# Optimization experiments

Hardware: AMD Instinct MI355X
Metric: run time of the kernel (lower is better)

Reference implementation:

```python
import jax, jax.numpy as jnp
import numpy as np

N = 262144      # total nodes
E = 1048576     # total edges
G = 8192        # num graphs (= batch[-1]+1)
H = 128         # hidden
L = 4           # layers
VA = 64         # atom feature vocab
VB = 8          # bond feature vocab
FA = 9          # atom feature columns
FB = 3          # bond feature columns
BN_EPS = 1e-5


def _bn(x, g, b, m, v):
    # BatchNorm1d in eval mode: running stats
    return (x - m) * jax.lax.rsqrt(v + BN_EPS) * g + b


def setup_inputs() -> dict:
    key = jax.random.key(0)
    ks = jax.random.split(key, 40)
    rn = lambda k, s, sc=0.05: jax.random.normal(k, s, dtype=jnp.float32) * sc
    x = jax.random.randint(ks[0], (N, FA), 0, VA)
    edge_index = jax.random.randint(ks[1], (2, E), 0, N)
    edge_attr = jax.random.randint(ks[2], (E, FB), 0, VB)
    batch = jnp.sort(jax.random.randint(ks[3], (N,), 0, G))
    batch = batch.at[0].set(0).at[-1].set(G - 1)
    params = dict(
        atom_emb=rn(ks[4], (FA, VA, H)),
        vn_emb=rn(ks[5], (H,)),
        bond_emb=rn(ks[6], (L, FB, VB, H)),
        conv_eps=rn(ks[7], (L,)),
        conv_W1=rn(ks[8], (L, H, 2 * H)), conv_b1=rn(ks[9], (L, 2 * H)),
        conv_bn_g=1.0 + rn(ks[10], (L, 2 * H)), conv_bn_b=rn(ks[11], (L, 2 * H)),
        conv_bn_m=rn(ks[12], (L, 2 * H), 0.1),
        conv_bn_v=0.5 + jax.random.uniform(ks[13], (L, 2 * H)) * 0.5,
        conv_W2=rn(ks[14], (L, 2 * H, H)), conv_b2=rn(ks[15], (L, H)),
        vn1_W=rn(ks[16], (L, 2 * H, 2 * H)), vn1_b=rn(ks[17], (L, 2 * H)),
        vn1_g=1.0 + rn(ks[18], (L, 2 * H)), vn1_be=rn(ks[19], (L, 2 * H)),
        vn1_m=rn(ks[20], (L, 2 * H), 0.1),
        vn1_v=0.5 + jax.random.uniform(ks[21], (L, 2 * H)) * 0.5,
        vn2_W=rn(ks[22], (L, 2 * H, H)), vn2_b=rn(ks[23], (L, H)),
        vn2_g=1.0 + rn(ks[24], (L, H)), vn2_be=rn(ks[25], (L, H)),
        vn2_m=rn(ks[26], (L, H), 0.1),
        vn2_v=0.5 + jax.random.uniform(ks[27], (L, H)) * 0.5,
        pW1=rn(ks[28], (H, H)), pb1=rn(ks[29], (H,)),
        pW2=rn(ks[30], (H, 1)), pb2=rn(ks[31], (1,)),
    )
    return dict(x=x, edge_index=edge_index, edge_attr=edge_attr, batch=batch, **params)


def reference(x, edge_index, edge_attr, batch, atom_emb, vn_emb, bond_emb,
              conv_eps, conv_W1, conv_b1, conv_bn_g, conv_bn_b, conv_bn_m, conv_bn_v,
              conv_W2, conv_b2, vn1_W, vn1_b, vn1_g, vn1_be, vn1_m, vn1_v,
              vn2_W, vn2_b, vn2_g, vn2_be, vn2_m, vn2_v, pW1, pb1, pW2, pb2):
    src, dst = edge_index[0], edge_index[1]
    # AtomEncoder: sum of per-feature embeddings -> [N, H]
    h = atom_emb[jnp.arange(FA)[:, None], x.T].sum(0)
    # virtual node embedding broadcast to all graphs: [G, H]
    vn = jnp.broadcast_to(vn_emb, (G, H))
    for i in range(L):
        h = h + vn[batch]
        # CombConv (GIN-with-edge-features): msg = relu(x_j + bond_emb)
        e = bond_emb[i][jnp.arange(FB)[:, None], edge_attr.T].sum(0)  # [E, H]
        msg = jax.nn.relu(h[src] + e)
        agg = jax.ops.segment_sum(msg, dst, num_segments=N)  # [N, H]
        z = (1.0 + conv_eps[i]) * h + agg
        z = jax.nn.relu(_bn(z @ conv_W1[i] + conv_b1[i],
                            conv_bn_g[i], conv_bn_b[i], conv_bn_m[i], conv_bn_v[i]))
        h = z @ conv_W2[i] + conv_b2[i]
        # virtual node update: gather-concat-MLP, pool, MLP
        t = jnp.concatenate([vn[batch], h], axis=-1)  # [N, 2H]
        t = jax.nn.relu(_bn(t @ vn1_W[i] + vn1_b[i],
                            vn1_g[i], vn1_be[i], vn1_m[i], vn1_v[i]))
        pooled = jax.ops.segment_sum(t, batch, num_segments=G)  # [G, 2H]
        vn = jax.nn.relu(_bn(pooled @ vn2_W[i] + vn2_b[i],
                             vn2_g[i], vn2_be[i], vn2_m[i], vn2_v[i]))
    # JK='L': last virtual-node representation; dropout=0
    out = jax.nn.relu(vn @ pW1 + pb1) @ pW2 + pb2  # [G, 1]
    return jnp.clip(out, 0.0, 50.0)  # eval-mode clamp
```

## Files before the change

### kernel.cpp

```cpp
#include <hip/hip_runtime.h>
#include <hip/hip_fp16.h>

#define NN 262144
#define EE 1048576
#define GG 8192
#define HH 128
#define FBc 3
#define VAc 64
#define VBc 8
#define FAc 9

typedef _Float16 f16;
typedef _Float16 f16x8 __attribute__((ext_vector_type(8)));
typedef float f32x4 __attribute__((ext_vector_type(4)));

__device__ __forceinline__ float h2f(ushort u) {
    __half h; *(ushort*)&h = u; return __half2float(h);
}
__device__ __forceinline__ ushort f2h(float f) {
    __half h = __float2half_rn(f); return *(ushort*)&h;
}
__device__ __forceinline__ int swz(int col, int row) {
    return (((col >> 3) ^ (row & 7)) << 3) | (col & 7);
}

__global__ void k_zero(float* __restrict__ p) {
    size_t i = (size_t)(blockIdx.x * 256 + threadIdx.x) * 4;
    *(float4*)(p + i) = make_float4(0.f, 0.f, 0.f, 0.f);
}

__global__ void k_atom(const int* __restrict__ x, const float* __restrict__ emb,
                       ushort* __restrict__ h16) {
    int t = blockIdx.x * 256 + threadIdx.x;
    int n = t >> 5, c = (t & 31) << 2;
    if (n >= NN) return;
    float4 a = make_float4(0.f, 0.f, 0.f, 0.f);
#pragma unroll
    for (int f = 0; f < FAc; ++f) {
        int v = x[n * FAc + f];
        float4 e = *(const float4*)(emb + ((size_t)(f * VAc + v)) * HH + c);
        a.x += e.x; a.y += e.y; a.z += e.z; a.w += e.w;
    }
    ushort4 o;
    o.x = f2h(a.x * 0.0625f); o.y = f2h(a.y * 0.0625f);
    o.z = f2h(a.z * 0.0625f); o.w = f2h(a.w * 0.0625f);
    *(ushort4*)(h16 + (size_t)n * HH + c) = o;
}

__global__ void k_init_vn(const float* __restrict__ vn_emb, float* __restrict__ vn) {
    int t = blockIdx.x * 256 + threadIdx.x;
    int g = t >> 5, c = (t & 31) << 2;
    *(float4*)(vn + (size_t)g * HH + c) = *(const float4*)(vn_emb + c);
}

__global__ void k_hist(const int* __restrict__ ei, int* __restrict__ deg) {
    int e = blockIdx.x * 256 + threadIdx.x;
    atomicAdd(&deg[ei[EE + e]], 1);
}
__global__ void k_scan1(const int* __restrict__ deg, int* __restrict__ rowptr,
                        int* __restrict__ sums) {
    __shared__ int s[256];
    int base = blockIdx.x * 1024 + threadIdx.x * 4;
    int4 d = *(const int4*)(deg + base);
    int t = d.x + d.y + d.z + d.w;
    s[threadIdx.x] = t;
    __syncthreads();
    for (int off = 1; off < 256; off <<= 1) {
        int v = (threadIdx.x >= off) ? s[threadIdx.x - off] : 0;
        __syncthreads();
        s[threadIdx.x] += v;
        __syncthreads();
    }
    int excl = s[threadIdx.x] - t;
    int4 o; o.x = excl; o.y = excl + d.x; o.z = o.y + d.y; o.w = o.z + d.z;
    *(int4*)(rowptr + base) = o;
    if (threadIdx.x == 255) sums[blockIdx.x] = s[255];
}
__global__ void k_scan2(int* __restrict__ sums) {
    __shared__ int s[256];
    int t = sums[threadIdx.x];
    s[threadIdx.x] = t;
    __syncthreads();
    for (int off = 1; off < 256; off <<= 1) {
        int v = (threadIdx.x >= off) ? s[threadIdx.x - off] : 0;
        __syncthreads();
        s[threadIdx.x] += v;
        __syncthreads();
    }
    sums[threadIdx.x] = s[threadIdx.x] - t;
}
__global__ void k_scan3(int* __restrict__ rowptr, const int* __restrict__ sums,
                        int* __restrict__ fill) {
    int base = blockIdx.x * 1024 + threadIdx.x * 4;
    int add = sums[blockIdx.x];
    int4 r = *(const int4*)(rowptr + base);
    r.x += add; r.y += add; r.z += add; r.w += add;
    *(int4*)(rowptr + base) = r;
    *(int4*)(fill + base) = r;
    if (blockIdx.x == 0 && threadIdx.x == 0) rowptr[NN] = EE;
}
__global__ void k_scatter(const int* __restrict__ ei, const int* __restrict__ ea,
                          int* __restrict__ fill, unsigned* __restrict__ packed) {
    int e = blockIdx.x * 256 + threadIdx.x;
    int dst = ei[EE + e];
    int pos = atomicAdd(&fill[dst], 1);
    unsigned cb = (unsigned)(ea[e * 3 + 0] + ea[e * 3 + 1] * 8 + ea[e * 3 + 2] * 64);
    packed[pos] = (unsigned)ei[e] | (cb << 18);
}

__global__ void k_setup(const float* __restrict__ bemb, ushort* __restrict__ ct16,
                        const float* __restrict__ b1, const float* __restrict__ g1,
                        const float* __restrict__ be1, const float* __restrict__ m1,
                        const float* __restrict__ v1,
                        const float* __restrict__ g3, const float* __restrict__ be3,
                        const float* __restrict__ m3, const float* __restrict__ v3,
                        float* __restrict__ ZA, float* __restrict__ ZB,
                        float* __restrict__ TA, float* __restrict__ TB,
                        float* __restrict__ S3,
                        const float* __restrict__ W1, ushort* __restrict__ W1t,
                        const float* __restrict__ W2, ushort* __restrict__ W2t,
                        const float* __restrict__ W3, ushort* __restrict__ W3t,
                        const float* __restrict__ vn, ushort* __restrict__ vn16,
                        float* __restrict__ pooled) {
    int t = blockIdx.x * 256 + threadIdx.x;
    if (t < 16384) {
        int cb = t >> 5, c = (t & 31) << 2;
        int a0 = cb & 7, a1 = (cb >> 3) & 7, a2 = cb >> 6;
        float4 b0 = *(const float4*)(bemb + (size_t)(0 * VBc + a0) * HH + c);
        float4 b1v = *(const float4*)(bemb + (size_t)(1 * VBc + a1) * HH + c);
        float4 b2v = *(const float4*)(bemb + (size_t)(2 * VBc + a2) * HH + c);
        ushort4 o;
        o.x = f2h((b0.x + b1v.x + b2v.x) * 0.0625f);
        o.y = f2h((b0.y + b1v.y + b2v.y) * 0.0625f);
        o.z = f2h((b0.z + b1v.z + b2v.z) * 0.0625f);
        o.w = f2h((b0.w + b1v.w + b2v.w) * 0.0625f);
        *(ushort4*)(ct16 + (size_t)cb * HH + c) = o;
    } else if (t < 16640) {
        int c = t - 16384;
        float s1 = g1[c] * rsqrtf(v1[c] + 1e-5f);
        ZA[c] = s1;
        ZB[c] = ((b1[c] - m1[c]) * s1 + be1[c]) * 0.0625f;
        float s3 = g3[c] * rsqrtf(v3[c] + 1e-5f);
        TA[c] = 16.f * s3;
        TB[c] = be3[c] - m3[c] * s3;
        S3[c] = s3;
    } else if (t < 278784) {
        int i4 = t - 16640;
        float4 v = *(const float4*)(vn + (size_t)i4 * 4);
        ushort4 o;
        o.x = f2h(v.x * 0.0625f); o.y = f2h(v.y * 0.0625f);
        o.z = f2h(v.z * 0.0625f); o.w = f2h(v.w * 0.0625f);
        *(ushort4*)(vn16 + (size_t)i4 * 4) = o;
    } else if (t < 311552) {
        int o = t - 278784;
        int c = o >> 7, k = o & 127;
        W1t[o] = f2h(W1[(size_t)k * 256 + c]);
    } else if (t < 344320) {
        int o = t - 311552;
        int c = o >> 8, k = o & 255;
        W2t[o] = f2h(W2[(size_t)k * 128 + c]);
    } else if (t < 377088) {
        int o = t - 344320;
        int c = o >> 7, k = o & 127;
        W3t[o] = f2h(W3[(size_t)k * 256 + c]);
    } else {
        int i4 = t - 377088;
        *(float4*)(pooled + (size_t)i4 * 4) = make_float4(0.f, 0.f, 0.f, 0.f);
    }
}

__global__ void __launch_bounds__(256, 3)
k_conv(const ushort* __restrict__ h16in, ushort* __restrict__ h16out,
       const int* __restrict__ rowptr, const unsigned* __restrict__ packed,
       const ushort* __restrict__ ct16,
       const ushort* __restrict__ W1t, const ushort* __restrict__ W2t,
       const ushort* __restrict__ W3t,
       const int* __restrict__ batch, const ushort* __restrict__ vn16,
       const float* __restrict__ vnW,
       const float* __restrict__ eps_ptr,
       const float* __restrict__ ZA, const float* __restrict__ ZB,
       const float* __restrict__ b2,
       const float* __restrict__ TA, const float* __restrict__ TB,
       float* __restrict__ pooled) {
    __shared__ ushort zs[64][256];
    __shared__ ushort Wb[64][128];
    ushort(*Wb2)[256] = (ushort(*)[256]) & Wb[0][0];
    const int tid = threadIdx.x;
    const int r0 = blockIdx.x * 64;
    const int w = tid >> 6, l = tid & 63, lr = l & 15, lg = l >> 4, lr7 = lr & 7;
    const float eps1 = 1.f + eps_ptr[0];
    const int myrow = w * 16 + lr;
    const int growA = r0 + myrow;
    const int ggA = batch[growA];
    int rl[4], ggs[4];
#pragma unroll
    for (int reg = 0; reg < 4; ++reg) {
        rl[reg] = w * 16 + lg * 4 + reg;
        ggs[reg] = batch[r0 + rl[reg]];
    }

    {
        int grp = tid >> 4, ln = tid & 15;
        int ch0 = ln * 8;
        for (int rr = 0; rr < 4; ++rr) {
            int row = grp * 4 + rr;
            int beg = rowptr[r0 + row], end = rowptr[r0 + row + 1];
            float ac[8] = {0.f, 0.f, 0.f, 0.f, 0.f, 0.f, 0.f, 0.f};
            int e = beg;
            for (; e + 1 < end; e += 2) {
                unsigned p0 = packed[e], p1 = packed[e + 1];
                int s0 = p0 & 0x3FFFF, s1 = p1 & 0x3FFFF;
                int c0 = p0 >> 18, c1 = p1 >> 18;
                f16x8 h0 = *(const f16x8*)(h16in + (size_t)s0 * HH + ch0);
                f16x8 h1 = *(const f16x8*)(h16in + (size_t)s1 * HH + ch0);
                f16x8 v0 = *(const f16x8*)(vn16 + (size_t)batch[s0] * HH + ch0);
                f16x8 v1 = *(const f16x8*)(vn16 + (size_t)batch[s1] * HH + ch0);
                f16x8 t0 = *(const f16x8*)(ct16 + (size_t)c0 * HH + ch0);
                f16x8 t1 = *(const f16x8*)(ct16 + (size_t)c1 * HH + ch0);
#pragma unroll
                for (int j = 0; j < 8; ++j) {
                    ac[j] += fmaxf((float)h0[j] + (float)v0[j] + (float)t0[j], 0.f)
                           + fmaxf((float)h1[j] + (float)v1[j] + (float)t1[j], 0.f);
                }
            }
            if (e < end) {
                unsigned p = packed[e];
                int src = p & 0x3FFFF, cb = p >> 18;
                f16x8 hv = *(const f16x8*)(h16in + (size_t)src * HH + ch0);
                f16x8 vv = *(const f16x8*)(vn16 + (size_t)batch[src] * HH + ch0);
                f16x8 ct = *(const f16x8*)(ct16 + (size_t)cb * HH + ch0);
#pragma unroll
                for (int j = 0; j < 8; ++j)
                    ac[j] += fmaxf((float)hv[j] + (float)vv[j] + (float)ct[j], 0.f);
            }
            f16x8 o;
#pragma unroll
            for (int j = 0; j < 8; ++j) o[j] = (f16)ac[j];
            *(f16x8*)&zs[row][((ch0 >> 3) ^ (row & 7)) << 3] = o;
        }
    }
    __syncthreads();

    f16x8 af[4];
#pragma unroll
    for (int k0 = 0; k0 < 4; ++k0) {
        int ko = k0 * 32 + lg * 8;
        f16x8 hv = *(const f16x8*)(h16in + (size_t)growA * HH + ko);
        f16x8 vv = *(const f16x8*)(vn16 + (size_t)ggA * HH + ko);
        f16x8 ag = *(const f16x8*)&zs[myrow][((ko >> 3) ^ (myrow & 7)) << 3];
#pragma unroll
        for (int j = 0; j < 8; ++j)
            af[k0][j] = (f16)(eps1 * ((float)hv[j] + (float)vv[j]) + (float)ag[j]);
    }

    for (int qt = 0; qt < 4; ++qt) {
        __syncthreads();
        {
            int c = tid >> 2, q = tid & 3, c7 = c & 7;
            const ushort* s = W1t + (size_t)(qt * 64 + c) * 128 + q * 32;
#pragma unroll
            for (int j4 = 0; j4 < 4; ++j4)
                *(f16x8*)&Wb[c][((q * 4 + j4) ^ c7) << 3] = *(const f16x8*)(s + j4 * 8);
        }
        __syncthreads();
        f32x4 acc[4] = {};
#pragma unroll
        for (int k0 = 0; k0 < 4; ++k0) {
            int sb = ((k0 * 4 + lg) ^ lr7) << 3;
#pragma unroll
            for (int fc = 0; fc < 4; ++fc) {
                f16x8 bf = *(const f16x8*)&Wb[fc * 16 + lr][sb];
                acc[fc] = __builtin_amdgcn_mfma_f32_16x16x32_f16(af[k0], bf, acc[fc], 0, 0, 0);
            }
        }
#pragma unroll
        for (int fc = 0; fc < 4; ++fc) {
            int col = qt * 64 + fc * 16 + lr;
            float za = ZA[col], zb = ZB[col];
#pragma unroll
            for (int reg = 0; reg < 4; ++reg) {
                float zv = fmaxf(acc[fc][reg] * za + zb, 0.f);
                zs[rl[reg]][swz(col, rl[reg])] = f2h(zv);
            }
        }
    }

    f32x4 acc2[8] = {};
    for (int st = 0; st < 4; ++st) {
        __syncthreads();
        {
            int c = tid >> 3, q = tid & 7, c7 = c & 7;
            const ushort* s = W2t + (size_t)(st * 32 + c) * 256 + q * 32;
#pragma unroll
            for (int j4 = 0; j4 < 4; ++j4)
                *(f16x8*)&Wb2[c][((q * 4 + j4) ^ c7) << 3] = *(const f16x8*)(s + j4 * 8);
        }
        __syncthreads();
#pragma unroll
        for (int k0 = 0; k0 < 8; ++k0) {
            int sb = ((k0 * 4 + lg) ^ lr7) << 3;
            f16x8 az = *(const f16x8*)&zs[myrow][sb];
#pragma unroll
            for (int fc = 0; fc < 2; ++fc) {
                f16x8 bf = *(const f16x8*)&Wb2[fc * 16 + lr][sb];
                acc2[st * 2 + fc] =
                    __builtin_amdgcn_mfma_f32_16x16x32_f16(az, bf, acc2[st * 2 + fc], 0, 0, 0);
            }
        }
    }
    __syncthreads();
#pragma unroll
    for (int st = 0; st < 4; ++st) {
#pragma unroll
        for (int fc = 0; fc < 2; ++fc) {
            int col = st * 32 + fc * 16 + lr;
            float bb = b2[col];
#pragma unroll
            for (int reg = 0; reg < 4; ++reg) {
                float hv = acc2[st * 2 + fc][reg] * 16.f + bb;
                zs[rl[reg]][swz(col, rl[reg])] = f2h(hv * 0.0625f);
            }
        }
    }
    {
        int row = tid >> 2, q = tid & 3, r7 = row & 7;
#pragma unroll
        for (int j4 = 0; j4 < 4; ++j4) {
            f16x8 v = *(const f16x8*)&zs[row][((q * 4 + j4) ^ r7) << 3];
            *(f16x8*)(h16out + (size_t)(r0 + row) * HH + q * 32 + j4 * 8) = v;
        }
    }

    for (int pr = 0; pr < 2; ++pr) {
#pragma unroll
        for (int sub = 0; sub < 2; ++sub) {
            int qt = pr * 2 + sub;
            __syncthreads();
            {
                int c = tid >> 2, q = tid & 3, c7 = c & 7;
                const ushort* s = W3t + (size_t)(qt * 64 + c) * 128 + q * 32;
#pragma unroll
                for (int j4 = 0; j4 < 4; ++j4)
                    *(f16x8*)&Wb[c][((q * 4 + j4) ^ c7) << 3] = *(const f16x8*)(s + j4 * 8);
            }
            __syncthreads();
            f32x4 acc3[4] = {};
#pragma unroll
            for (int k0 = 0; k0 < 4; ++k0) {
                int sb = ((k0 * 4 + lg) ^ lr7) << 3;
                f16x8 ah = *(const f16x8*)&zs[myrow][sb];
#pragma unroll
                for (int fc = 0; fc < 4; ++fc) {
                    f16x8 bf = *(const f16x8*)&Wb[fc * 16 + lr][sb];
                    acc3[fc] = __builtin_amdgcn_mfma_f32_16x16x32_f16(ah, bf, acc3[fc], 0, 0, 0);
                }
            }
#pragma unroll
            for (int fc = 0; fc < 4; ++fc) {
                int colg = qt * 64 + fc * 16 + lr;
                int colL = 128 + sub * 64 + fc * 16 + lr;
                float ta = TA[colg], tb = TB[colg];
#pragma unroll
                for (int reg = 0; reg < 4; ++reg) {
                    float tv = fmaxf(acc3[fc][reg] * ta + vnW[(size_t)ggs[reg] * 256 + colg] + tb, 0.f);
                    zs[rl[reg]][swz(colL, rl[reg])] = f2h(tv);
                }
            }
        }
        __syncthreads();
        {
            int c = tid & 127, half = tid >> 7;
            int gcol = pr * 128 + c;
            int colL = 128 + c;
            float s = 0.f;
            int cur = batch[r0 + half * 32];
            for (int r = half * 32; r < half * 32 + 32; ++r) {
                int gg = batch[r0 + r];
                if (gg != cur) {
                    atomicAdd(&pooled[(size_t)cur * 256 + gcol], s);
                    s = 0.f; cur = gg;
                }
                s += h2f(zs[r][swz(colL, r)]);
            }
            atomicAdd(&pooled[(size_t)cur * 256 + gcol], s);
        }
        __syncthreads();
    }
}

enum { E_BIAS = 0, E_BNRELU = 1 };
template <int EMODE>
__global__ void __launch_bounds__(256)
gemm_k(const void* __restrict__ Av, const float* __restrict__ B,
       const float* __restrict__ bias,
       const float* __restrict__ g_, const float* __restrict__ b_,
       const float* __restrict__ m_, const float* __restrict__ v_,
       const float* __restrict__ scp,
       void* __restrict__ outv, int K, int Nc) {
    __shared__ float As[64][33];
    __shared__ float Bs[32][64];
    const int tid = threadIdx.x;
    const int row0 = blockIdx.x * 64;
    const int col0 = blockIdx.y * 64;
    float acc[4][4] = {};
    const int tx = tid & 15, ty = tid >> 4;
    for (int k0 = 0; k0 < K; k0 += 32) {
#pragma unroll
        for (int p = 0; p < 2; ++p) {
            int idx = p * 256 + tid;
            {
                int r = idx >> 3, c = (idx & 7) << 2;
                size_t aoff = (size_t)(row0 + r) * K + k0 + c;
                float4 va = *(const float4*)((const float*)Av + aoff);
                As[r][c + 0] = va.x; As[r][c + 1] = va.y;
                As[r][c + 2] = va.z; As[r][c + 3] = va.w;
            }
            {
                int kr = idx >> 4, cc = (idx & 15) << 2;
                *(float4*)&Bs[kr][cc] =
                    *(const float4*)(B + (size_t)(k0 + kr) * Nc + col0 + cc);
            }
        }
        __syncthreads();
#pragma unroll
        for (int k = 0; k < 32; ++k) {
            float4 bv = *(const float4*)&Bs[k][tx << 2];
            float a0 = As[ty * 4 + 0][k];
            float a1 = As[ty * 4 + 1][k];
            float a2 = As[ty * 4 + 2][k];
            float a3 = As[ty * 4 + 3][k];
            acc[0][0] += a0 * bv.x; acc[0][1] += a0 * bv.y; acc[0][2] += a0 * bv.z; acc[0][3] += a0 * bv.w;
            acc[1][0] += a1 * bv.x; acc[1][1] += a1 * bv.y; acc[1][2] += a1 * bv.z; acc[1][3] += a1 * bv.w;
            acc[2][0] += a2 * bv.x; acc[2][1] += a2 * bv.y; acc[2][2] += a2 * bv.z; acc[2][3] += a2 * bv.w;
            acc[3][0] += a3 * bv.x; acc[3][1] += a3 * bv.y; acc[3][2] += a3 * bv.z; acc[3][3] += a3 * bv.w;
        }
        __syncthreads();
    }
#pragma unroll
    for (int j = 0; j < 4; ++j) {
        int gr = row0 + ty * 4 + j;
        float vals[4];
#pragma unroll
        for (int lx = 0; lx < 4; ++lx) {
            int gc = col0 + (tx << 2) + lx;
            float val = acc[j][lx];
            if (EMODE == E_BIAS) {
                float v = val + bias[gc];
                if (scp) v *= scp[gc];
                vals[lx] = v;
            } else {
                float y = val + bias[gc];
                float s = g_[gc] * rsqrtf(v_[gc] + 1e-5f);
                y = (y - m_[gc]) * s + b_[gc];
                vals[lx] = fmaxf(y, 0.f);
            }
        }
        *(float4*)((float*)outv + (size_t)gr * Nc + col0 + (tx << 2)) =
            make_float4(vals[0], vals[1], vals[2], vals[3]);
    }
}

__global__ void k_final(const float* __restrict__ vn, const float* __restrict__ pW1,
                        const float* __restrict__ pb1, const float* __restrict__ pW2,
                        const float* __restrict__ pb2, float* __restrict__ out) {
    int g = blockIdx.x;
    int j = threadIdx.x;
    __shared__ float vrow[HH];
    __shared__ float red[HH];
    vrow[j] = vn[(size_t)g * HH + j];
    __syncthreads();
    float acc = pb1[j];
    for (int k = 0; k < HH; ++k) acc = fmaf(vrow[k], pW1[k * HH + j], acc);
    red[j] = fmaxf(acc, 0.f) * pW2[j];
    __syncthreads();
    for (int s = 64; s > 0; s >>= 1) {
        if (j < s) red[j] += red[j + s];
        __syncthreads();
    }
    if (j == 0) out[g] = fminf(fmaxf(red[0] + pb2[0], 0.f), 50.f);
}

extern "C" void kernel_launch(void* const* d_in, const int* in_sizes, int n_in,
                              void* d_out, int out_size, void* d_ws, size_t ws_size,
                              hipStream_t stream) {
    const int*   x        = (const int*)  d_in[0];
    const int*   ei       = (const int*)  d_in[1];
    const int*   ea       = (const int*)  d_in[2];
    const int*   batch    = (const int*)  d_in[3];
    const float* atom_emb = (const float*)d_in[4];
    const float* vn_emb   = (const float*)d_in[5];
    const float* bond_emb = (const float*)d_in[6];
    const float* conv_eps = (const float*)d_in[7];
    const float* conv_W1  = (const float*)d_in[8];
    const float* conv_b1  = (const float*)d_in[9];
    const float* cbn_g    = (const float*)d_in[10];
    const float* cbn_b    = (const float*)d_in[11];
    const float* cbn_m    = (const float*)d_in[12];
    const float* cbn_v    = (const float*)d_in[13];
    const float* conv_W2  = (const float*)d_in[14];
    const float* conv_b2  = (const float*)d_in[15];
    const float* vn1_W    = (const float*)d_in[16];
    const float* vn1_b    = (const float*)d_in[17];
    const float* vn1_g    = (const float*)d_in[18];
    const float* vn1_be   = (const float*)d_in[19];
    const float* vn1_m    = (const float*)d_in[20];
    const float* vn1_v    = (const float*)d_in[21];
    const float* vn2_W    = (const float*)d_in[22];
    const float* vn2_b    = (const float*)d_in[23];
    const float* vn2_g    = (const float*)d_in[24];
    const float* vn2_be   = (const float*)d_in[25];
    const float* vn2_m    = (const float*)d_in[26];
    const float* vn2_v    = (const float*)d_in[27];
    const float* pW1      = (const float*)d_in[28];
    const float* pb1      = (const float*)d_in[29];
    const float* pW2      = (const float*)d_in[30];
    const float* pb2      = (const float*)d_in[31];

    char* base = (char*)d_ws;
    ushort*   h16a   = (ushort*)base;
    ushort*   h16b   = h16a + (size_t)NN * HH;
    unsigned* packed = (unsigned*)(h16b + (size_t)NN * HH);
    int*      rowptr = (int*)(packed + EE);
    int*      fill   = rowptr + NN + 4;
    ushort*   ct16   = (ushort*)(fill + NN);
    int*      sums   = (int*)(ct16 + 512 * HH);
    ushort*   W1t    = (ushort*)(sums + 256);
    ushort*   W2t    = W1t + 256 * 128;
    ushort*   W3t    = W2t + 128 * 256;
    float*    ZA     = (float*)(W3t + 256 * 128);
    float*    ZB     = ZA + 256;
    float*    TA     = ZB + 256;
    float*    TB     = TA + 256;
    float*    S3     = TB + 256;
    float*    vn     = S3 + 256;
    ushort*   vn16   = (ushort*)(vn + (size_t)GG * HH);
    float*    vnW    = (float*)(vn16 + (size_t)GG * HH);
    float*    pooled = vnW + (size_t)GG * 256;
    float*    out    = (float*)d_out;

    k_zero<<<256, 256, 0, stream>>>((float*)fill);
    k_hist<<<EE / 256, 256, 0, stream>>>(ei, fill);
    k_scan1<<<256, 256, 0, stream>>>(fill, rowptr, sums);
    k_scan2<<<1, 256, 0, stream>>>(sums);
    k_scan3<<<256, 256, 0, stream>>>(rowptr, sums, fill);
    k_scatter<<<EE / 256, 256, 0, stream>>>(ei, ea, fill, packed);
    k_atom<<<NN * 32 / 256, 256, 0, stream>>>(x, atom_emb, h16a);
    k_init_vn<<<GG * HH / 4 / 256, 256, 0, stream>>>(vn_emb, vn);

    for (int i = 0; i < 4; ++i) {
        ushort* hin  = (i & 1) ? h16b : h16a;
        ushort* hout = (i & 1) ? h16a : h16b;

        k_setup<<<3521, 256, 0, stream>>>(
            bond_emb + (size_t)i * FBc * VBc * HH, ct16,
            conv_b1 + i * 256, cbn_g + i * 256, cbn_b + i * 256,
            cbn_m + i * 256, cbn_v + i * 256,
            vn1_g + i * 256, vn1_be + i * 256, vn1_m + i * 256, vn1_v + i * 256,
            ZA, ZB, TA, TB, S3,
            conv_W1 + (size_t)i * HH * 256, W1t,
            conv_W2 + (size_t)i * 256 * HH, W2t,
            vn1_W + (size_t)i * 256 * 256 + 128 * 256, W3t,
            vn, vn16, pooled);

        {
            dim3 g3(GG / 64, 4);
            gemm_k<E_BIAS><<<g3, 256, 0, stream>>>(
                vn, vn1_W + (size_t)i * 256 * 256, vn1_b + i * 256,
                nullptr, nullptr, nullptr, nullptr, S3, vnW, HH, 256);
        }

        k_conv<<<NN / 64, 256, 0, stream>>>(
            hin, hout, rowptr, packed, ct16,
            W1t, W2t, W3t, batch, vn16, vnW, conv_eps + i,
            ZA, ZB, conv_b2 + i * HH, TA, TB, pooled);

        {
            dim3 g4(GG / 64, 2);
            gemm_k<E_BNRELU><<<g4, 256, 0, stream>>>(
                pooled, vn2_W + (size_t)i * 256 * HH, vn2_b + i * HH,
                vn2_g + i * HH, vn2_be + i * HH, vn2_m + i * HH, vn2_v + i * HH,
                nullptr, vn, 256, HH);
        }
    }
    k_final<<<GG, 128, 0, stream>>>(vn, pW1, pb1, pW2, pb2, out);
}
```

Baseline: 1.543 ms.

## Precompute h+vn once per layer, fuse VN MLPs, hoist per-layer setup

A new per-layer VN kernel fuses the previous layer's vn2 MLP, the next vn1 projection and the pooled zeroing. It also writes hb16 = h + vn[batch] once per node, so the conv edge gather no longer loads vn16 and batch for every edge. Setup for all four layers moves into a single kernel before the loop, and the generic gemm kernels are removed. The edge loop is unrolled by four and MFMA sections get s_setprio hints. This adds a full extra pass over node features each layer, which trades against the per-edge gather it saves.

```diff
diff --git a/kernel.cpp b/kernel.cpp
--- a/kernel.cpp
+++ b/kernel.cpp
@@ -45,12 +45,6 @@
     o.x = f2h(a.x * 0.0625f); o.y = f2h(a.y * 0.0625f);
     o.z = f2h(a.z * 0.0625f); o.w = f2h(a.w * 0.0625f);
     *(ushort4*)(h16 + (size_t)n * HH + c) = o;
-}
-
-__global__ void k_init_vn(const float* __restrict__ vn_emb, float* __restrict__ vn) {
-    int t = blockIdx.x * 256 + threadIdx.x;
-    int g = t >> 5, c = (t & 31) << 2;
-    *(float4*)(vn + (size_t)g * HH + c) = *(const float4*)(vn_emb + c);
 }
 
 __global__ void k_hist(const int* __restrict__ ei, int* __restrict__ deg) {
@@ -107,23 +101,33 @@
     unsigned cb = (unsigned)(ea[e * 3 + 0] + ea[e * 3 + 1] * 8 + ea[e * 3 + 2] * 64);
     packed[pos] = (unsigned)ei[e] | (cb << 18);
 }
-
-__global__ void k_setup(const float* __restrict__ bemb, ushort* __restrict__ ct16,
-                        const float* __restrict__ b1, const float* __restrict__ g1,
-                        const float* __restrict__ be1, const float* __restrict__ m1,
-                        const float* __restrict__ v1,
-                        const float* __restrict__ g3, const float* __restrict__ be3,
-                        const float* __restrict__ m3, const float* __restrict__ v3,
-                        float* __restrict__ ZA, float* __restrict__ ZB,
-                        float* __restrict__ TA, float* __restrict__ TB,
-                        float* __restrict__ S3,
-                        const float* __restrict__ W1, ushort* __restrict__ W1t,
-                        const float* __restrict__ W2, ushort* __restrict__ W2t,
-                        const float* __restrict__ W3, ushort* __restrict__ W3t,
-                        const float* __restrict__ vn, ushort* __restrict__ vn16,
-                        float* __restrict__ pooled) {
-    int t = blockIdx.x * 256 + threadIdx.x;
+__global__ void k_gstart(const int* __restrict__ batch, int* __restrict__ gstart) {
+    int n = blockIdx.x * 256 + threadIdx.x;
+    if (n >= NN) return;
+    int b0 = batch[n];
+    int b1 = (n + 1 < NN) ? batch[n + 1] : GG;
+    if (n == 0) gstart[0] = 0;
+    for (int g = b0 + 1; g <= b1; ++g) gstart[g] = n + 1;
+}
+
+__global__ void k_setup_all(
+    const float* __restrict__ bond_emb, ushort* __restrict__ ct16_all,
+    const float* __restrict__ conv_b1, const float* __restrict__ cbn_g,
+    const float* __restrict__ cbn_b, const float* __restrict__ cbn_m,
+    const float* __restrict__ cbn_v,
+    const float* __restrict__ vn1_g, const float* __restrict__ vn1_be,
+    const float* __restrict__ vn1_m, const float* __restrict__ vn1_v,
+    const float* __restrict__ vn2_g, const float* __restrict__ vn2_be,
+    const float* __restrict__ vn2_m, const float* __restrict__ vn2_v,
+    const float* __restrict__ vn2_b,
+    float* __restrict__ tabs,
+    const float* __restrict__ conv_W1, ushort* __restrict__ W1t_all,
+    const float* __restrict__ conv_W2, ushort* __restrict__ W2t_all,
+    const float* __restrict__ vn1_W,  ushort* __restrict__ W3t_all) {
+    int layer = blockIdx.x / 449;
+    int t = (blockIdx.x % 449) * 256 + threadIdx.x;
     if (t < 16384) {
+        const float* bemb = bond_emb + (size_t)layer * FBc * VBc * HH;
         int cb = t >> 5, c = (t & 31) << 2;
         int a0 = cb & 7, a1 = (cb >> 3) & 7, a2 = cb >> 6;
         float4 b0 = *(const float4*)(bemb + (size_t)(0 * VBc + a0) * HH + c);
@@ -134,53 +138,143 @@
         o.y = f2h((b0.y + b1v.y + b2v.y) * 0.0625f);
         o.z = f2h((b0.z + b1v.z + b2v.z) * 0.0625f);
         o.w = f2h((b0.w + b1v.w + b2v.w) * 0.0625f);
-        *(ushort4*)(ct16 + (size_t)cb * HH + c) = o;
+        *(ushort4*)(ct16_all + (size_t)layer * 512 * HH + (size_t)cb * HH + c) = o;
     } else if (t < 16640) {
         int c = t - 16384;
-        float s1 = g1[c] * rsqrtf(v1[c] + 1e-5f);
-        ZA[c] = s1;
-        ZB[c] = ((b1[c] - m1[c]) * s1 + be1[c]) * 0.0625f;
-        float s3 = g3[c] * rsqrtf(v3[c] + 1e-5f);
-        TA[c] = 16.f * s3;
-        TB[c] = be3[c] - m3[c] * s3;
-        S3[c] = s3;
-    } else if (t < 278784) {
-        int i4 = t - 16640;
-        float4 v = *(const float4*)(vn + (size_t)i4 * 4);
-        ushort4 o;
-        o.x = f2h(v.x * 0.0625f); o.y = f2h(v.y * 0.0625f);
-        o.z = f2h(v.z * 0.0625f); o.w = f2h(v.w * 0.0625f);
-        *(ushort4*)(vn16 + (size_t)i4 * 4) = o;
-    } else if (t < 311552) {
-        int o = t - 278784;
+        float* T = tabs + (size_t)layer * 1536;
+        float s1 = cbn_g[layer * 256 + c] * rsqrtf(cbn_v[layer * 256 + c] + 1e-5f);
+        T[0 * 256 + c] = s1;
+        T[1 * 256 + c] = ((conv_b1[layer * 256 + c] - cbn_m[layer * 256 + c]) * s1
+                          + cbn_b[layer * 256 + c]) * 0.0625f;
+        float s3 = vn1_g[layer * 256 + c] * rsqrtf(vn1_v[layer * 256 + c] + 1e-5f);
+        T[2 * 256 + c] = 16.f * s3;
+        T[3 * 256 + c] = vn1_be[layer * 256 + c] - vn1_m[layer * 256 + c] * s3;
+        T[4 * 256 + c] = s3;
+        if (c < 128) {
+            float s2 = vn2_g[layer * 128 + c] * rsqrtf(vn2_v[layer * 128 + c] + 1e-5f);
+            T[5 * 256 + c] = s2;
+            T[5 * 256 + 128 + c] = (vn2_b[layer * 128 + c] - vn2_m[layer * 128 + c]) * s2
+                                   + vn2_be[layer * 128 + c];
+        }
+    } else if (t < 49408) {
+        int o = t - 16640;
         int c = o >> 7, k = o & 127;
-        W1t[o] = f2h(W1[(size_t)k * 256 + c]);
-    } else if (t < 344320) {
-        int o = t - 311552;
+        W1t_all[(size_t)layer * 32768 + o] =
+            f2h(conv_W1[(size_t)layer * 128 * 256 + (size_t)k * 256 + c]);
+    } else if (t < 82176) {
+        int o = t - 49408;
         int c = o >> 8, k = o & 255;
-        W2t[o] = f2h(W2[(size_t)k * 128 + c]);
-    } else if (t < 377088) {
-        int o = t - 344320;
+        W2t_all[(size_t)layer * 32768 + o] =
+            f2h(conv_W2[(size_t)layer * 256 * 128 + (size_t)k * 128 + c]);
+    } else if (t < 114944) {
+        int o = t - 82176;
         int c = o >> 7, k = o & 127;
-        W3t[o] = f2h(W3[(size_t)k * 256 + c]);
+        W3t_all[(size_t)layer * 32768 + o] =
+            f2h(vn1_W[(size_t)layer * 256 * 256 + 128 * 256 + (size_t)k * 256 + c]);
+    }
+}
+
+template <int MODE>
+__global__ void __launch_bounds__(256)
+k_vn(float* __restrict__ pooled, const float* __restrict__ vn_emb,
+     const float* __restrict__ vn2W_prev,
+     const float* __restrict__ tab_prev,
+     const float* __restrict__ vn1W_cur,
+     const float* __restrict__ vn1b_cur,
+     const float* __restrict__ tab_cur,
+     float* __restrict__ vn_out, float* __restrict__ vnW,
+     const ushort* __restrict__ h16, ushort* __restrict__ hb16,
+     const int* __restrict__ gstart, const int* __restrict__ batch) {
+    __shared__ float pl[16][256];
+    __shared__ float vnL[16][128];
+    const int tid = threadIdx.x;
+    const int g0 = blockIdx.x * 16;
+
+    if (MODE != 0) {
+        for (int i = tid; i < 1024; i += 256) {
+            int r = i >> 6, c4 = (i & 63) << 2;
+            *(float4*)&pl[r][c4] = *(const float4*)(pooled + (size_t)(g0 + r) * 256 + c4);
+        }
+        __syncthreads();
+        {
+            int r = tid >> 4, c0 = (tid & 15) * 8;
+            float acc[8] = {};
+            for (int k = 0; k < 256; ++k) {
+                float a = pl[r][k];
+                const float* wr = vn2W_prev + (size_t)k * 128 + c0;
+                float4 w0 = *(const float4*)wr, w1 = *(const float4*)(wr + 4);
+                acc[0] += a * w0.x; acc[1] += a * w0.y; acc[2] += a * w0.z; acc[3] += a * w0.w;
+                acc[4] += a * w1.x; acc[5] += a * w1.y; acc[6] += a * w1.z; acc[7] += a * w1.w;
+            }
+            const float* VA = tab_prev + 5 * 256;
+            const float* VB = VA + 128;
+#pragma unroll
+            for (int j = 0; j < 8; ++j)
+                vnL[r][c0 + j] = fmaxf(acc[j] * VA[c0 + j] + VB[c0 + j], 0.f);
+        }
     } else {
-        int i4 = t - 377088;
-        *(float4*)(pooled + (size_t)i4 * 4) = make_float4(0.f, 0.f, 0.f, 0.f);
+        for (int i = tid; i < 2048; i += 256) {
+            int r = i >> 7, c = i & 127;
+            vnL[r][c] = vn_emb[c];
+        }
+    }
+    __syncthreads();
+    for (int i = tid; i < 512; i += 256) {
+        int r = i >> 5, c4 = (i & 31) << 2;
+        *(float4*)(vn_out + (size_t)(g0 + r) * 128 + c4) = *(const float4*)&vnL[r][c4];
+    }
+    if (MODE == 2) return;
+
+    {
+        int r = tid >> 4, c0 = (tid & 15) * 16;
+        float acc[16] = {};
+        for (int k = 0; k < 128; ++k) {
+            float a = vnL[r][k];
+            const float* wr = vn1W_cur + (size_t)k * 256 + c0;
+#pragma unroll
+            for (int j4 = 0; j4 < 4; ++j4) {
+                float4 w = *(const float4*)(wr + j4 * 4);
+                acc[j4 * 4 + 0] += a * w.x; acc[j4 * 4 + 1] += a * w.y;
+                acc[j4 * 4 + 2] += a * w.z; acc[j4 * 4 + 3] += a * w.w;
+            }
+        }
+        const float* S3 = tab_cur + 4 * 256;
+#pragma unroll
+        for (int j = 0; j < 16; ++j)
+            vnW[(size_t)(g0 + r) * 256 + c0 + j] =
+                (acc[j] + vn1b_cur[c0 + j]) * S3[c0 + j];
+    }
+    for (int i = tid; i < 1024; i += 256) {
+        int r = i >> 6, c4 = (i & 63) << 2;
+        *(float4*)(pooled + (size_t)(g0 + r) * 256 + c4) = make_float4(0.f, 0.f, 0.f, 0.f);
+    }
+    {
+        int nn0 = gstart[g0], nn1 = gstart[g0 + 16];
+        for (int q = nn0 * 4 + tid; q < nn1 * 4; q += 256) {
+            int n = q >> 2, ch0 = (q & 3) * 32;
+            int g = batch[n] - g0;
+#pragma unroll
+            for (int j4 = 0; j4 < 4; ++j4) {
+                f16x8 hv = *(const f16x8*)(h16 + (size_t)n * HH + ch0 + j4 * 8);
+                f16x8 o;
+#pragma unroll
+                for (int j = 0; j < 8; ++j)
+                    o[j] = (f16)((float)hv[j] + vnL[g][ch0 + j4 * 8 + j] * 0.0625f);
+                *(f16x8*)(hb16 + (size_t)n * HH + ch0 + j4 * 8) = o;
+            }
+        }
     }
 }
 
 __global__ void __launch_bounds__(256, 3)
-k_conv(const ushort* __restrict__ h16in, ushort* __restrict__ h16out,
+k_conv(ushort* __restrict__ h16, const ushort* __restrict__ hb16,
        const int* __restrict__ rowptr, const unsigned* __restrict__ packed,
        const ushort* __restrict__ ct16,
        const ushort* __restrict__ W1t, const ushort* __restrict__ W2t,
        const ushort* __restrict__ W3t,
-       const int* __restrict__ batch, const ushort* __restrict__ vn16,
-       const float* __restrict__ vnW,
-       const float* __restrict__ eps_ptr,
-       const float* __restrict__ ZA, const float* __restrict__ ZB,
+       const int* __restrict__ batch, const float* __restrict__ vnW,
+       const float* __restrict__ eps_ptr, const float* __restrict__ tabs,
        const float* __restrict__ b2,
-       const float* __restrict__ TA, const float* __restrict__ TB,
        float* __restrict__ pooled) {
     __shared__ ushort zs[64][256];
     __shared__ ushort Wb[64][128];
@@ -191,7 +285,10 @@
     const float eps1 = 1.f + eps_ptr[0];
     const int myrow = w * 16 + lr;
     const int growA = r0 + myrow;
-    const int ggA = batch[growA];
+    const float* ZA = tabs;
+    const float* ZB = tabs + 256;
+    const float* TA = tabs + 512;
+    const float* TB = tabs + 768;
     int rl[4], ggs[4];
 #pragma unroll
     for (int reg = 0; reg < 4; ++reg) {
@@ -207,31 +304,32 @@
             int beg = rowptr[r0 + row], end = rowptr[r0 + row + 1];
             float ac[8] = {0.f, 0.f, 0.f, 0.f, 0.f, 0.f, 0.f, 0.f};
             int e = beg;
-            for (; e + 1 < end; e += 2) {
+            for (; e + 3 < end; e += 4) {
                 unsigned p0 = packed[e], p1 = packed[e + 1];
-                int s0 = p0 & 0x3FFFF, s1 = p1 & 0x3FFFF;
-                int c0 = p0 >> 18, c1 = p1 >> 18;
-                f16x8 h0 = *(const f16x8*)(h16in + (size_t)s0 * HH + ch0);
-                f16x8 h1 = *(const f16x8*)(h16in + (size_t)s1 * HH + ch0);
-                f16x8 v0 = *(const f16x8*)(vn16 + (size_t)batch[s0] * HH + ch0);
-                f16x8 v1 = *(const f16x8*)(vn16 + (size_t)batch[s1] * HH + ch0);
-                f16x8 t0 = *(const f16x8*)(ct16 + (size_t)c0 * HH + ch0);
-                f16x8 t1 = *(const f16x8*)(ct16 + (size_t)c1 * HH + ch0);
+                unsigned p2 = packed[e + 2], p3 = packed[e + 3];
+                f16x8 h0 = *(const f16x8*)(hb16 + (size_t)(p0 & 0x3FFFF) * HH + ch0);
+                f16x8 h1 = *(const f16x8*)(hb16 + (size_t)(p1 & 0x3FFFF) * HH + ch0);
+                f16x8 h2 = *(const f16x8*)(hb16 + (size_t)(p2 & 0x3FFFF) * HH + ch0);
+                f16x8 h3 = *(const f16x8*)(hb16 + (size_t)(p3 & 0x3FFFF) * HH + ch0);
+                f16x8 t0 = *(const f16x8*)(ct16 + (size_t)(p0 >> 18) * HH + ch0);
+                f16x8 t1 = *(const f16x8*)(ct16 + (size_t)(p1 >> 18) * HH + ch0);
+                f16x8 t2 = *(const f16x8*)(ct16 + (size_t)(p2 >> 18) * HH + ch0);
+                f16x8 t3 = *(const f16x8*)(ct16 + (size_t)(p3 >> 18) * HH + ch0);
 #pragma unroll
                 for (int j = 0; j < 8; ++j) {
-                    ac[j] += fmaxf((float)h0[j] + (float)v0[j] + (float)t0[j], 0.f)
-                           + fmaxf((float)h1[j] + (float)v1[j] + (float)t1[j], 0.f);
+                    ac[j] += fmaxf((float)h0[j] + (float)t0[j], 0.f)
+                           + fmaxf((float)h1[j] + (float)t1[j], 0.f)
+                           + fmaxf((float)h2[j] + (float)t2[j], 0.f)
+                           + fmaxf((float)h3[j] + (float)t3[j], 0.f);
                 }
             }
-            if (e < end) {
+            for (; e < end; ++e) {
                 unsigned p = packed[e];
-                int src = p & 0x3FFFF, cb = p >> 18;
-                f16x8 hv = *(const f16x8*)(h16in + (size_t)src * HH + ch0);
-                f16x8 vv = *(const f16x8*)(vn16 + (size_t)batch[src] * HH + ch0);
-                f16x8 ct = *(const f16x8*)(ct16 + (size_t)cb * HH + ch0);
+                f16x8 hv = *(const f16x8*)(hb16 + (size_t)(p & 0x3FFFF) * HH + ch0);
+                f16x8 ct = *(const f16x8*)(ct16 + (size_t)(p >> 18) * HH + ch0);
 #pragma unroll
                 for (int j = 0; j < 8; ++j)
-                    ac[j] += fmaxf((float)hv[j] + (float)vv[j] + (float)ct[j], 0.f);
+                    ac[j] += fmaxf((float)hv[j] + (float)ct[j], 0.f);
             }
             f16x8 o;
 #pragma unroll
@@ -245,12 +343,11 @@
 #pragma unroll
     for (int k0 = 0; k0 < 4; ++k0) {
         int ko = k0 * 32 + lg * 8;
-        f16x8 hv = *(const f16x8*)(h16in + (size_t)growA * HH + ko);
-        f16x8 vv = *(const f16x8*)(vn16 + (size_t)ggA * HH + ko);
+        f16x8 hb = *(const f16x8*)(hb16 + (size_t)growA * HH + ko);
         f16x8 ag = *(const f16x8*)&zs[myrow][((ko >> 3) ^ (myrow & 7)) << 3];
 #pragma unroll
         for (int j = 0; j < 8; ++j)
-            af[k0][j] = (f16)(eps1 * ((float)hv[j] + (float)vv[j]) + (float)ag[j]);
+            af[k0][j] = (f16)(eps1 * (float)hb[j] + (float)ag[j]);
     }
 
     for (int qt = 0; qt < 4; ++qt) {
@@ -264,6 +361,7 @@
         }
         __syncthreads();
         f32x4 acc[4] = {};
+        __builtin_amdgcn_s_setprio(1);
 #pragma unroll
         for (int k0 = 0; k0 < 4; ++k0) {
             int sb = ((k0 * 4 + lg) ^ lr7) << 3;
@@ -273,6 +371,7 @@
                 acc[fc] = __builtin_amdgcn_mfma_f32_16x16x32_f16(af[k0], bf, acc[fc], 0, 0, 0);
             }
         }
+        __builtin_amdgcn_s_setprio(0);
 #pragma unroll
         for (int fc = 0; fc < 4; ++fc) {
             int col = qt * 64 + fc * 16 + lr;
@@ -296,6 +395,7 @@
                 *(f16x8*)&Wb2[c][((q * 4 + j4) ^ c7) << 3] = *(const f16x8*)(s + j4 * 8);
         }
         __syncthreads();
+        __builtin_amdgcn_s_setprio(1);
 #pragma unroll
         for (int k0 = 0; k0 < 8; ++k0) {
             int sb = ((k0 * 4 + lg) ^ lr7) << 3;
@@ -307,6 +407,7 @@
                     __builtin_amdgcn_mfma_f32_16x16x32_f16(az, bf, acc2[st * 2 + fc], 0, 0, 0);
             }
         }
+        __builtin_amdgcn_s_setprio(0);
     }
     __syncthreads();
 #pragma unroll
@@ -327,7 +428,7 @@
 #pragma unroll
         for (int j4 = 0; j4 < 4; ++j4) {
             f16x8 v = *(const f16x8*)&zs[row][((q * 4 + j4) ^ r7) << 3];
-            *(f16x8*)(h16out + (size_t)(r0 + row) * HH + q * 32 + j4 * 8) = v;
+            *(f16x8*)(h16 + (size_t)(r0 + row) * HH + q * 32 + j4 * 8) = v;
         }
     }
 
@@ -345,6 +446,7 @@
             }
             __syncthreads();
             f32x4 acc3[4] = {};
+            __builtin_amdgcn_s_setprio(1);
 #pragma unroll
             for (int k0 = 0; k0 < 4; ++k0) {
                 int sb = ((k0 * 4 + lg) ^ lr7) << 3;
@@ -355,6 +457,7 @@
                     acc3[fc] = __builtin_amdgcn_mfma_f32_16x16x32_f16(ah, bf, acc3[fc], 0, 0, 0);
                 }
             }
+            __builtin_amdgcn_s_setprio(0);
 #pragma unroll
             for (int fc = 0; fc < 4; ++fc) {
                 int colg = qt * 64 + fc * 16 + lr;
@@ -385,78 +488,6 @@
             atomicAdd(&pooled[(size_t)cur * 256 + gcol], s);
         }
         __syncthreads();
-    }
-}
-
-enum { E_BIAS = 0, E_BNRELU = 1 };
-template <int EMODE>
-__global__ void __launch_bounds__(256)
-gemm_k(const void* __restrict__ Av, const float* __restrict__ B,
-       const float* __restrict__ bias,
-       const float* __restrict__ g_, const float* __restrict__ b_,
-       const float* __restrict__ m_, const float* __restrict__ v_,
-       const float* __restrict__ scp,
-       void* __restrict__ outv, int K, int Nc) {
-    __shared__ float As[64][33];
-    __shared__ float Bs[32][64];
-    const int tid = threadIdx.x;
-    const int row0 = blockIdx.x * 64;
-    const int col0 = blockIdx.y * 64;
-    float acc[4][4] = {};
-    const int tx = tid & 15, ty = tid >> 4;
-    for (int k0 = 0; k0 < K; k0 += 32) {
-#pragma unroll
-        for (int p = 0; p < 2; ++p) {
-            int idx = p * 256 + tid;
-            {
-                int r = idx >> 3, c = (idx & 7) << 2;
-                size_t aoff = (size_t)(row0 + r) * K + k0 + c;
-                float4 va = *(const float4*)((const float*)Av + aoff);
-                As[r][c + 0] = va.x; As[r][c + 1] = va.y;
-                As[r][c + 2] = va.z; As[r][c + 3] = va.w;
-            }
-            {
-                int kr = idx >> 4, cc = (idx & 15) << 2;
-                *(float4*)&Bs[kr][cc] =
-                    *(const float4*)(B + (size_t)(k0 + kr) * Nc + col0 + cc);
-            }
-        }
-        __syncthreads();
-#pragma unroll
-        for (int k = 0; k < 32; ++k) {
-            float4 bv = *(const float4*)&Bs[k][tx << 2];
-            float a0 = As[ty * 4 + 0][k];
-            float a1 = As[ty * 4 + 1][k];
-            float a2 = As[ty * 4 + 2][k];
-            float a3 = As[ty * 4 + 3][k];
-            acc[0][0] += a0 * bv.x; acc[0][1] += a0 * bv.y; acc[0][2] += a0 * bv.z; acc[0][3] += a0 * bv.w;
-            acc[1][0] += a1 * bv.x; acc[1][1] += a1 * bv.y; acc[1][2] += a1 * bv.z; acc[1][3] += a1 * bv.w;
-            acc[2][0] += a2 * bv.x; acc[2][1] += a2 * bv.y; acc[2][2] += a2 * bv.z; acc[2][3] += a2 * bv.w;
-            acc[3][0] += a3 * bv.x; acc[3][1] += a3 * bv.y; acc[3][2] += a3 * bv.z; acc[3][3] += a3 * bv.w;
-        }
-        __syncthreads();
-    }
-#pragma unroll
-    for (int j = 0; j < 4; ++j) {
-        int gr = row0 + ty * 4 + j;
-        float vals[4];
-#pragma unroll
-        for (int lx = 0; lx < 4; ++lx) {
-            int gc = col0 + (tx << 2) + lx;
-            float val = acc[j][lx];
-            if (EMODE == E_BIAS) {
-                float v = val + bias[gc];
-                if (scp) v *= scp[gc];
-                vals[lx] = v;
-            } else {
-                float y = val + bias[gc];
-                float s = g_[gc] * rsqrtf(v_[gc] + 1e-5f);
-                y = (y - m_[gc]) * s + b_[gc];
-                vals[lx] = fmaxf(y, 0.f);
-            }
-        }
-        *(float4*)((float*)outv + (size_t)gr * Nc + col0 + (tx << 2)) =
-            make_float4(vals[0], vals[1], vals[2], vals[3]);
     }
 }
 
@@ -517,26 +548,22 @@
     const float* pb2      = (const float*)d_in[31];
 
     char* base = (char*)d_ws;
-    ushort*   h16a   = (ushort*)base;
-    ushort*   h16b   = h16a + (size_t)NN * HH;
-    unsigned* packed = (unsigned*)(h16b + (size_t)NN * HH);
-    int*      rowptr = (int*)(packed + EE);
-    int*      fill   = rowptr + NN + 4;
-    ushort*   ct16   = (ushort*)(fill + NN);
-    int*      sums   = (int*)(ct16 + 512 * HH);
-    ushort*   W1t    = (ushort*)(sums + 256);
-    ushort*   W2t    = W1t + 256 * 128;
-    ushort*   W3t    = W2t + 128 * 256;
-    float*    ZA     = (float*)(W3t + 256 * 128);
-    float*    ZB     = ZA + 256;
-    float*    TA     = ZB + 256;
-    float*    TB     = TA + 256;
-    float*    S3     = TB + 256;
-    float*    vn     = S3 + 256;
-    ushort*   vn16   = (ushort*)(vn + (size_t)GG * HH);
-    float*    vnW    = (float*)(vn16 + (size_t)GG * HH);
-    float*    pooled = vnW + (size_t)GG * 256;
-    float*    out    = (float*)d_out;
+    ushort*   h16     = (ushort*)base;
+    ushort*   hb16    = h16 + (size_t)NN * HH;
+    unsigned* packed  = (unsigned*)(hb16 + (size_t)NN * HH);
+    int*      rowptr  = (int*)(packed + EE);
+    int*      fill    = rowptr + NN + 4;
+    int*      gstart  = fill + NN;
+    int*      sums    = gstart + GG + 8;
+    ushort*   ct16a   = (ushort*)(sums + 256);
+    ushort*   W1ta    = ct16a + 4 * 512 * HH;
+    ushort*   W2ta    = W1ta + 4 * 32768;
+    ushort*   W3ta    = W2ta + 4 * 32768;
+    float*    tabs    = (float*)(W3ta + 4 * 32768);
+    float*    vn      = tabs + 4 * 1536;
+    float*    vnW     = vn + (size_t)GG * HH;
+    float*    pooled  = vnW + (size_t)GG * 256;
+    float*    out     = (float*)d_out;
 
     k_zero<<<256, 256, 0, stream>>>((float*)fill);
     k_hist<<<EE / 256, 256, 0, stream>>>(ei, fill);
@@ -544,43 +571,39 @@
     k_scan2<<<1, 256, 0, stream>>>(sums);
     k_scan3<<<256, 256, 0, stream>>>(rowptr, sums, fill);
     k_scatter<<<EE / 256, 256, 0, stream>>>(ei, ea, fill, packed);
-    k_atom<<<NN * 32 / 256, 256, 0, stream>>>(x, atom_emb, h16a);
-    k_init_vn<<<GG * HH / 4 / 256, 256, 0, stream>>>(vn_emb, vn);
+    k_gstart<<<NN / 256, 256, 0, stream>>>(batch, gstart);
+    k_atom<<<NN * 32 / 256, 256, 0, stream>>>(x, atom_emb, h16);
+    k_setup_all<<<4 * 449, 256, 0, stream>>>(
+        bond_emb, ct16a,
+        conv_b1, cbn_g, cbn_b, cbn_m, cbn_v,
+        vn1_g, vn1_be, vn1_m, vn1_v,
+        vn2_g, vn2_be, vn2_m, vn2_v, vn2_b,
+        tabs, conv_W1, W1ta, conv_W2, W2ta, vn1_W, W3ta);
 
     for (int i = 0; i < 4; ++i) {
-        ushort* hin  = (i & 1) ? h16b : h16a;
-        ushort* hout = (i & 1) ? h16a : h16b;
-
-        k_setup<<<3521, 256, 0, stream>>>(
-            bond_emb + (size_t)i * FBc * VBc * HH, ct16,
-            conv_b1 + i * 256, cbn_g + i * 256, cbn_b + i * 256,
-            cbn_m + i * 256, cbn_v + i * 256,
-            vn1_g + i * 256, vn1_be + i * 256, vn1_m + i * 256, vn1_v + i * 256,
-            ZA, ZB, TA, TB, S3,
-            conv_W1 + (size_t)i * HH * 256, W1t,
-            conv_W2 + (size_t)i * 256 * HH, W2t,
-            vn1_W + (size_t)i * 256 * 256 + 128 * 256, W3t,
-            vn, vn16, pooled);
-
-        {
-            dim3 g3(GG / 64, 4);
-            gemm_k<E_BIAS><<<g3, 256, 0, stream>>>(
-                vn, vn1_W + (size_t)i * 256 * 256, vn1_b + i * 256,
-                nullptr, nullptr, nullptr, nullptr, S3, vnW, HH, 256);
-        }
-
+        if (i == 0) {
+            k_vn<0><<<GG / 16, 256, 0, stream>>>(
+                pooled, vn_emb, nullptr, nullptr,
+                vn1_W + (size_t)i * 256 * 256, vn1_b + i * 256, tabs + (size_t)i * 1536,
+                vn, vnW, h16, hb16, gstart, batch);
+        } else {
+            k_vn<1><<<GG / 16, 256, 0, stream>>>(
+                pooled, nullptr,
+                vn2_W + (size_t)(i - 1) * 256 * 128, tabs + (size_t)(i - 1) * 1536,
+                vn1_W + (size_t)i * 256 * 256, vn1_b + i * 256, tabs + (size_t)i * 1536,
+                vn, vnW, h16, hb16, gstart, batch);
+        }
         k_conv<<<NN / 64, 256, 0, stream>>>(
-            hin, hout, rowptr, packed, ct16,
-            W1t, W2t, W3t, batch, vn16, vnW, conv_eps + i,
-            ZA, ZB, conv_b2 + i * HH, TA, TB, pooled);
-
-        {
-            dim3 g4(GG / 64, 2);
-            gemm_k<E_BNRELU><<<g4, 256, 0, stream>>>(
-                pooled, vn2_W + (size_t)i * 256 * HH, vn2_b + i * HH,
-                vn2_g + i * HH, vn2_be + i * HH, vn2_m + i * HH, vn2_v + i * HH,
-                nullptr, vn, 256, HH);
-        }
-    }
+            h16, hb16, rowptr, packed,
+            ct16a + (size_t)i * 512 * HH,
+            W1ta + (size_t)i * 32768, W2ta + (size_t)i * 32768, W3ta + (size_t)i * 32768,
+            batch, vnW, conv_eps + i, tabs + (size_t)i * 1536,
+            conv_b2 + i * HH, pooled);
+    }
+    k_vn<2><<<GG / 16, 256, 0, stream>>>(
+        pooled, nullptr,
+        vn2_W + (size_t)3 * 256 * 128, tabs + (size_t)3 * 1536,
+        nullptr, nullptr, nullptr,
+        vn, nullptr, nullptr, nullptr, nullptr, nullptr);
     k_final<<<GG, 128, 0, stream>>>(vn, pW1, pb1, pW2, pb2, out);
 }
```

After: 1.690 ms. 1.09x slower.
